# Kernel tuning notes

Measured on AMD Instinct MI355X. Metric: run time of the kernel, lower is better.

## Reference

```python
import jax, jax.numpy as jnp
import numpy as np

SIG = 10
C = 0.0
STD = 1.0
N_ATOMS = 21
N_TRAIN = 8192
DESC = N_ATOMS * (N_ATOMS - 1) // 2  # 210
M = 64


def setup_inputs() -> dict:
    key = jax.random.key(0)
    k1, k2, k3 = jax.random.split(key, 3)
    Rs = jax.random.normal(k1, (M, N_ATOMS, 3), dtype=jnp.float32)
    xs_train = jax.random.uniform(k2, (N_TRAIN, DESC), dtype=jnp.float32)
    Jx_alphas = jax.random.normal(k3, (N_TRAIN, DESC), dtype=jnp.float32)
    return {"Rs": Rs, "xs_train": xs_train, "Jx_alphas": Jx_alphas}


def reference(Rs, xs_train, Jx_alphas):
    sig = SIG
    q = np.sqrt(5.0) / sig
    n = N_ATOMS
    # pairwise atom displacements / distances: [M, n, n, 3], [M, n, n]
    diffs = Rs[:, :, None, :] - Rs[:, None, :, :]
    dists = jnp.linalg.norm(diffs, axis=-1)
    eye = jnp.eye(n, dtype=bool)
    dists = jnp.where(eye, jnp.inf, dists)  # kill diagonal
    i, j = np.tril_indices(n, k=-1)
    xs = 1.0 / dists[:, i, j]                       # [M, D] inverse-distance descriptor
    x_diffs = q * xs[:, None, :] - q * xs_train     # [M, T, D]
    x_dists = jnp.linalg.norm(x_diffs, axis=-1)     # [M, T]
    exp_xs = (5.0 / (3.0 * sig ** 2)) * jnp.exp(-x_dists)
    dot = jnp.einsum('mtd,td->mt', x_diffs, Jx_alphas)
    exp_xs_1 = exp_xs * (1.0 + x_dists)
    F1s_x = jnp.einsum('mt,mtd->md', exp_xs * dot, x_diffs)  # [M, D]
    F2s_x = exp_xs_1 @ Jx_alphas                              # [M, D]
    Fs_x = (F1s_x - F2s_x) * STD
    # expand_tril: scatter D lower-tri values to symmetric [M, n, n], zero diag
    full = jnp.zeros((Fs_x.shape[0], n, n), dtype=Fs_x.dtype)
    full = full.at[:, i, j].set(Fs_x).at[:, j, i].set(Fs_x)
    Fs = jnp.einsum('mab,mabc->mac', full / dists ** 3, diffs)  # diag: 0/inf -> 0
    Es = jnp.sum(exp_xs_1 * dot, axis=-1) / q
    Es = C + Es * STD
    return Es, Fs
```

## Files before the change

kernel.cpp:

```cpp
#include <hip/hip_runtime.h>
#include <math.h>

#define NA   21
#define NM   64
#define ND   210
#define DP   224
#define NT   8192
#define NCH  28
#define KS2  32

#define QC 0.22360679774997896f
#define KE 0.016666666666666666f

typedef short bf8 __attribute__((ext_vector_type(8)));
typedef float f4  __attribute__((ext_vector_type(4)));

#define O_XF   0u
#define O_JF   917504u
#define O_XFT  1835008u
#define O_JFT  2752512u
#define O_W1   3670016u
#define O_E1   3932160u
#define O_AF   4194304u
#define O_QG   4201472u
#define O_NTT  4215808u
#define O_CJ   4224000u
#define O_NX   4232192u
#define O_PB   4261056u
#define O_ESP  5178560u
#define O_WAP  5211328u

__device__ __forceinline__ unsigned short f2bf(float f) {
    unsigned u = __float_as_uint(f);
    u += 0x7fffu + ((u >> 16) & 1u);
    return (unsigned short)(u >> 16);
}
__device__ __forceinline__ float bf2f(unsigned short h) {
    return __uint_as_float((unsigned)h << 16);
}

__device__ __forceinline__ void d_to_ij(int d, int& i, int& j) {
    int ii = (int)((1.0f + sqrtf(1.0f + 8.0f * (float)d)) * 0.5f);
    while (ii * (ii - 1) / 2 > d) --ii;
    while ((ii + 1) * ii / 2 <= d) ++ii;
    i = ii;
    j = d - ii * (ii - 1) / 2;
}

__global__ __launch_bounds__(256) void k_prep(
    const float* __restrict__ Rs, const float* __restrict__ xs,
    const float* __restrict__ Jx,
    unsigned short* __restrict__ Xf, unsigned short* __restrict__ Jf,
    unsigned short* __restrict__ XfT, unsigned short* __restrict__ JfT,
    unsigned short* __restrict__ Af, float* __restrict__ qxsG,
    float* __restrict__ nx, float* __restrict__ nt, float* __restrict__ cJ) {
    const int b = blockIdx.x, tid = threadIdx.x;
    __shared__ float lds[2 * 16 * 210];

    if (b < 512) {
        const int t0 = b * 16;
        const float4* sx = (const float4*)(xs + (size_t)t0 * ND);
        const float4* sj = (const float4*)(Jx + (size_t)t0 * ND);
#pragma unroll
        for (int k = 0; k < 4; ++k) {
            const int i = k * 256 + tid;
            if (i < 840) {
                ((float4*)lds)[i] = sx[i];
                ((float4*)(lds + 3360))[i] = sj[i];
            }
        }
        __syncthreads();
#pragma unroll
        for (int k = 0; k < 7; ++k) {
            const int idx = k * 256 + tid;
            if (idx < 896) {
                const int arr = idx / 448;
                const int rem = idx - arr * 448;
                const int kq = rem >> 4, colt = rem & 15;
                const float* src = lds + arr * 3360 + colt * 210;
                const float sc = arr ? 1.0f : QC;
                union { unsigned short us[8]; uint4 v; } u;
#pragma unroll
                for (int i = 0; i < 8; ++i) {
                    const int d = kq * 8 + i;
                    u.us[i] = (d < ND) ? f2bf(sc * src[d]) : (unsigned short)0;
                }
                *(uint4*)((arr ? Jf : Xf) + ((size_t)(b * NCH + kq) * 16 + colt) * 8) = u.v;
            } else {
                const int idx2 = idx - 896;
                const int arr = idx2 / 448;
                const int rem = idx2 - arr * 448;
                const int dtile = rem >> 5;
                const int rem2 = rem & 31;
                const int tql = rem2 >> 4, col = rem2 & 15;
                const int d = dtile * 16 + col;
                const float* src = lds + arr * 3360 + tql * 8 * 210;
                const float sc = arr ? 1.0f : QC;
                union { unsigned short us[8]; uint4 v; } u;
#pragma unroll
                for (int i = 0; i < 8; ++i)
                    u.us[i] = (d < ND) ? f2bf(sc * src[i * 210 + d])
                                       : (unsigned short)0;
                const size_t off = ((size_t)(dtile * 1024 + b * 2 + tql) * 16 + col) * 8;
                *(uint4*)((arr ? JfT : XfT) + off) = u.v;
            }
        }
        const int tt = tid >> 4, l = tid & 15;
        const float* xr = lds + tt * 210;
        const float* jr = lds + 3360 + tt * 210;
        float sn = 0.0f, sc2 = 0.0f;
        for (int c = l; c < ND; c += 16) {
            float x = bf2f(f2bf(QC * xr[c]));
            float j = bf2f(f2bf(jr[c]));
            sn = fmaf(x, x, sn);
            sc2 = fmaf(x, j, sc2);
        }
#pragma unroll
        for (int off = 1; off < 16; off <<= 1) {
            sn += __shfl_xor(sn, off);
            sc2 += __shfl_xor(sc2, off);
        }
        if (l == 0) {
            nt[t0 + tt] = sn;
            cJ[t0 + tt] = sc2;
        }
    } else {
        const int m = b - 512;
        float* R = lds;
        float* red = lds + 64;
        if (tid < NA * 3) R[tid] = Rs[m * NA * 3 + tid];
        __syncthreads();
        float local = 0.0f;
        if (tid < DP) {
            float vr = 0.0f;
            unsigned short hv = 0;
            if (tid < ND) {
                int i, j; d_to_ij(tid, i, j);
                float dx = R[i * 3] - R[j * 3];
                float dy = R[i * 3 + 1] - R[j * 3 + 1];
                float dz = R[i * 3 + 2] - R[j * 3 + 2];
                float v = QC / sqrtf(dx * dx + dy * dy + dz * dz);
                hv = f2bf(v);
                vr = bf2f(hv);
            }
            Af[(((m >> 4) * NCH + (tid >> 3)) * 16 + (m & 15)) * 8 + (tid & 7)] = hv;
            qxsG[(tid >> 2) * 256 + m * 4 + (tid & 3)] = vr;
            local = vr * vr;
        }
        red[tid] = local;
        __syncthreads();
        for (int s = 128; s > 0; s >>= 1) {
            if (tid < s) red[tid] += red[tid + s];
            __syncthreads();
        }
        if (tid == 0) nx[m] = red[0];
    }
}

__global__ __launch_bounds__(256) void k_stage1(
    const unsigned short* __restrict__ Af, const unsigned short* __restrict__ Xf,
    const unsigned short* __restrict__ Jf, const float* __restrict__ nt,
    const float* __restrict__ cJ, const float* __restrict__ nx,
    unsigned short* __restrict__ w1f, unsigned short* __restrict__ e1f,
    float* __restrict__ EsPart, float* __restrict__ WaPart) {
    const int tid = threadIdx.x;
    const int lane = tid & 63;
    const int w = tid >> 6;
    const int col = lane & 15, quad = lane >> 4;
    const int ttile = blockIdx.x;
    __shared__ float Dw[64][17];
    __shared__ float De[64][17];

    const unsigned short* ap = Af + ((size_t)(w * NCH + quad) * 16 + col) * 8;
    const unsigned short* xp = Xf + ((size_t)(ttile * NCH + quad) * 16 + col) * 8;
    const unsigned short* jp = Jf + ((size_t)(ttile * NCH + quad) * 16 + col) * 8;

    bf8 af[7];
#pragma unroll
    for (int kc = 0; kc < 7; ++kc) af[kc] = *(const bf8*)(ap + kc * 512);

    bf8 bx[2], bj[2];
    bx[0] = *(const bf8*)xp;
    bj[0] = *(const bf8*)jp;
    bx[1] = *(const bf8*)(xp + 512);
    bj[1] = *(const bf8*)(jp + 512);

    f4 c1 = {0.f, 0.f, 0.f, 0.f};
    f4 c2 = {0.f, 0.f, 0.f, 0.f};
#pragma unroll
    for (int kc = 0; kc < 7; ++kc) {
        const int s = kc & 1;
        c1 = __builtin_amdgcn_mfma_f32_16x16x32_bf16(af[kc], bx[s], c1, 0, 0, 0);
        c2 = __builtin_amdgcn_mfma_f32_16x16x32_bf16(af[kc], bj[s], c2, 0, 0, 0);
        if (kc < 5) {
            bx[s] = *(const bf8*)(xp + (kc + 2) * 512);
            bj[s] = *(const bf8*)(jp + (kc + 2) * 512);
        }
    }

    const int t = ttile * 16 + col;
    const float ntv = nt[t], cjv = cJ[t];
    float esA[4], wlA[4];
#pragma unroll
    for (int r = 0; r < 4; ++r) {
        const int m = w * 16 + quad * 4 + r;
        float sq = fmaxf(nx[m] - 2.0f * c1[r] + ntv, 0.0f);
        float xd = sqrtf(sq);
        float e = KE * expf(-xd);
        float dotv = c2[r] - cjv;
        float wv = e * dotv;
        float ev = e * (1.0f + xd);
        Dw[m][col] = wv;
        De[m][col] = ev;
        esA[r] = ev * dotv;
        wlA[r] = wv;
    }
    __syncthreads();
    {
        const int aidx = tid >> 7;
        const int c = tid & 127;
        const int mtile = c >> 5, tql = (c >> 4) & 1, colm = c & 15;
        const float* srcD = aidx ? &De[0][0] : &Dw[0][0];
        unsigned short* dst = aidx ? e1f : w1f;
        const int m = mtile * 16 + colm;
        union { unsigned short us[8]; uint4 v; } u;
#pragma unroll
        for (int i = 0; i < 8; ++i) u.us[i] = f2bf(srcD[m * 17 + tql * 8 + i]);
        const size_t off = ((size_t)(mtile * 1024 + ttile * 2 + tql) * 16 + colm) * 8;
        *(uint4*)(dst + off) = u.v;
    }
#pragma unroll
    for (int r = 0; r < 4; ++r) {
        float e = esA[r], wl = wlA[r];
#pragma unroll
        for (int off = 1; off < 16; off <<= 1) {
            e += __shfl_xor(e, off);
            wl += __shfl_xor(wl, off);
        }
        if (col == 0) {
            const int m = w * 16 + quad * 4 + r;
            EsPart[(size_t)m * 512 + ttile] = e;
            WaPart[(size_t)m * 512 + ttile] = wl;
        }
    }
}

__global__ __launch_bounds__(256) void k_stage2(
    const unsigned short* __restrict__ w1f, const unsigned short* __restrict__ e1f,
    const unsigned short* __restrict__ XfT, const unsigned short* __restrict__ JfT,
    float* __restrict__ Pbuf) {
    const int tid = threadIdx.x;
    const int lane = tid & 63;
    const int w = tid >> 6;
    const int col = lane & 15, quad = lane >> 4;
    const int dt = blockIdx.x;
    const int by = blockIdx.y;

    const unsigned short* awp = w1f + ((size_t)(w * 1024 + by * 32 + quad) * 16 + col) * 8;
    const unsigned short* aep = e1f + ((size_t)(w * 1024 + by * 32 + quad) * 16 + col) * 8;
    const unsigned short* bxp = XfT + ((size_t)(dt * 1024 + by * 32 + quad) * 16 + col) * 8;
    const unsigned short* bjp = JfT + ((size_t)(dt * 1024 + by * 32 + quad) * 16 + col) * 8;

    bf8 aw[2], ae[2], bx[2], bj[2];
    aw[0] = *(const bf8*)awp;         ae[0] = *(const bf8*)aep;
    bx[0] = *(const bf8*)bxp;         bj[0] = *(const bf8*)bjp;
    aw[1] = *(const bf8*)(awp + 512); ae[1] = *(const bf8*)(aep + 512);
    bx[1] = *(const bf8*)(bxp + 512); bj[1] = *(const bf8*)(bjp + 512);

    f4 dA = {0.f, 0.f, 0.f, 0.f};
    f4 dB = {0.f, 0.f, 0.f, 0.f};
#pragma unroll
    for (int kk = 0; kk < 8; ++kk) {
        const int s = kk & 1;
        dA = __builtin_amdgcn_mfma_f32_16x16x32_bf16(aw[s], bx[s], dA, 0, 0, 0);
        dB = __builtin_amdgcn_mfma_f32_16x16x32_bf16(ae[s], bj[s], dB, 0, 0, 0);
        if (kk < 6) {
            aw[s] = *(const bf8*)(awp + (kk + 2) * 512);
            ae[s] = *(const bf8*)(aep + (kk + 2) * 512);
            bx[s] = *(const bf8*)(bxp + (kk + 2) * 512);
            bj[s] = *(const bf8*)(bjp + (kk + 2) * 512);
        }
    }
    float* p = Pbuf + (size_t)by * 28672 + dt * 16 + col;
#pragma unroll
    for (int r = 0; r < 4; ++r) {
        const int m = w * 16 + quad * 4 + r;
        p[m * DP] = dA[r];
        p[14336 + m * DP] = dB[r];
    }
}

__global__ void k_final(const float* __restrict__ Rs, const float* __restrict__ qxsG,
                        const float* __restrict__ Pbuf, const float* __restrict__ EsPart,
                        const float* __restrict__ WaPart, float* __restrict__ out) {
    int m = blockIdx.x, tid = threadIdx.x;
    __shared__ float R[NA * 3];
    __shared__ float Ff[NA][NA];
    __shared__ float redE[256];
    __shared__ float redW[256];
    __shared__ float ABs[DP];
    if (tid < NA * 3) R[tid] = Rs[m * NA * 3 + tid];
    if (tid < NA) Ff[tid][tid] = 0.0f;
    if (tid < DP) {
        const float* p0 = Pbuf + (size_t)m * DP + tid;
        float s1 = 0.0f, s2 = 0.0f;
#pragma unroll
        for (int ks = 0; ks < KS2; ++ks) {
            s1 += p0[(size_t)ks * 28672];
            s2 += p0[(size_t)ks * 28672 + 14336];
        }
        ABs[tid] = s1 + s2;
    }
    {
        const float2 ep = ((const float2*)(EsPart + (size_t)m * 512))[tid];
        const float2 wp = ((const float2*)(WaPart + (size_t)m * 512))[tid];
        redE[tid] = ep.x + ep.y;
        redW[tid] = wp.x + wp.y;
    }
    __syncthreads();
    for (int s = 128; s > 0; s >>= 1) {
        if (tid < s) {
            redE[tid] += redE[tid + s];
            redW[tid] += redW[tid + s];
        }
        __syncthreads();
    }
    const float Wa = redW[0];
    if (tid < ND) {
        int i, j; d_to_ij(tid, i, j);
        float dx = R[i * 3] - R[j * 3];
        float dy = R[i * 3 + 1] - R[j * 3 + 1];
        float dz = R[i * 3 + 2] - R[j * 3 + 2];
        float dist2 = dx * dx + dy * dy + dz * dz;
        float fsx = qxsG[(tid >> 2) * 256 + m * 4 + (tid & 3)] * Wa - ABs[tid];
        float f = fsx / (dist2 * sqrtf(dist2));
        Ff[i][j] = f;
        Ff[j][i] = f;
    }
    __syncthreads();
    if (tid < NA * 3) {
        int a = tid / 3, c = tid % 3;
        float s = 0.0f;
        for (int b = 0; b < NA; ++b) {
            if (b == a) continue;
            s += Ff[a][b] * (R[a * 3 + c] - R[b * 3 + c]);
        }
        out[NM + m * NA * 3 + tid] = s;
    }
    if (tid == 0) out[m] = redE[0] / QC;
}

extern "C" void kernel_launch(void* const* d_in, const int* in_sizes, int n_in,
                              void* d_out, int out_size, void* d_ws, size_t ws_size,
                              hipStream_t stream) {
    const float* Rs = (const float*)d_in[0];
    const float* xs_train = (const float*)d_in[1];
    const float* Jx_alphas = (const float*)d_in[2];
    float* out = (float*)d_out;
    float* ws = (float*)d_ws;

    unsigned short* Xf  = (unsigned short*)(ws + O_XF);
    unsigned short* Jf  = (unsigned short*)(ws + O_JF);
    unsigned short* XfT = (unsigned short*)(ws + O_XFT);
    unsigned short* JfT = (unsigned short*)(ws + O_JFT);
    unsigned short* w1f = (unsigned short*)(ws + O_W1);
    unsigned short* e1f = (unsigned short*)(ws + O_E1);
    unsigned short* Af  = (unsigned short*)(ws + O_AF);
    float* qxsG   = ws + O_QG;
    float* nt     = ws + O_NTT;
    float* cJ     = ws + O_CJ;
    float* nx     = ws + O_NX;
    float* Pbuf   = ws + O_PB;
    float* EsPart = ws + O_ESP;
    float* WaPart = ws + O_WAP;

    k_prep<<<576, 256, 0, stream>>>(Rs, xs_train, Jx_alphas, Xf, Jf, XfT, JfT,
                                    Af, qxsG, nx, nt, cJ);
    k_stage1<<<512, 256, 0, stream>>>(Af, Xf, Jf, nt, cJ, nx, w1f, e1f, EsPart, WaPart);
    k_stage2<<<dim3(14, KS2), 256, 0, stream>>>(w1f, e1f, XfT, JfT, Pbuf);
    k_final<<<NM, 256, 0, stream>>>(Rs, qxsG, Pbuf, EsPart, WaPart, out);
}
```

Before: 92.13 us.

## Fuse prep and stage1 kernels, recomputing descriptor fragments per block in LDS

Merges the preprocessing kernel into stage1. Each block recomputes the full 64-molecule inverse-distance A-fragments and its own train-tile bf16 B-fragments in shared memory, instead of writing them to global workspace and reading them back. This removes one kernel launch and the global round trip for Xf/Jf/Af/nt/cJ/nx, and k_final now recomputes qxs itself. The cost is redundant work: every one of the 512 blocks reads all of Rs and recomputes 64x224 inverse distances, and the larger LDS footprint may lower occupancy.

Result: slower. 105.3 us (+14.2%).

```diff
diff --git a/kernel.cpp b/kernel.cpp
--- a/kernel.cpp
+++ b/kernel.cpp
@@ -15,17 +15,10 @@
 typedef short bf8 __attribute__((ext_vector_type(8)));
 typedef float f4  __attribute__((ext_vector_type(4)));
 
-#define O_XF   0u
-#define O_JF   917504u
 #define O_XFT  1835008u
 #define O_JFT  2752512u
 #define O_W1   3670016u
 #define O_E1   3932160u
-#define O_AF   4194304u
-#define O_QG   4201472u
-#define O_NTT  4215808u
-#define O_CJ   4224000u
-#define O_NX   4232192u
 #define O_PB   4261056u
 #define O_ESP  5178560u
 #define O_WAP  5211328u
@@ -47,120 +40,10 @@
     j = d - ii * (ii - 1) / 2;
 }
 
-__global__ __launch_bounds__(256) void k_prep(
+__global__ __launch_bounds__(256) void k_mega(
     const float* __restrict__ Rs, const float* __restrict__ xs,
     const float* __restrict__ Jx,
-    unsigned short* __restrict__ Xf, unsigned short* __restrict__ Jf,
     unsigned short* __restrict__ XfT, unsigned short* __restrict__ JfT,
-    unsigned short* __restrict__ Af, float* __restrict__ qxsG,
-    float* __restrict__ nx, float* __restrict__ nt, float* __restrict__ cJ) {
-    const int b = blockIdx.x, tid = threadIdx.x;
-    __shared__ float lds[2 * 16 * 210];
-
-    if (b < 512) {
-        const int t0 = b * 16;
-        const float4* sx = (const float4*)(xs + (size_t)t0 * ND);
-        const float4* sj = (const float4*)(Jx + (size_t)t0 * ND);
-#pragma unroll
-        for (int k = 0; k < 4; ++k) {
-            const int i = k * 256 + tid;
-            if (i < 840) {
-                ((float4*)lds)[i] = sx[i];
-                ((float4*)(lds + 3360))[i] = sj[i];
-            }
-        }
-        __syncthreads();
-#pragma unroll
-        for (int k = 0; k < 7; ++k) {
-            const int idx = k * 256 + tid;
-            if (idx < 896) {
-                const int arr = idx / 448;
-                const int rem = idx - arr * 448;
-                const int kq = rem >> 4, colt = rem & 15;
-                const float* src = lds + arr * 3360 + colt * 210;
-                const float sc = arr ? 1.0f : QC;
-                union { unsigned short us[8]; uint4 v; } u;
-#pragma unroll
-                for (int i = 0; i < 8; ++i) {
-                    const int d = kq * 8 + i;
-                    u.us[i] = (d < ND) ? f2bf(sc * src[d]) : (unsigned short)0;
-                }
-                *(uint4*)((arr ? Jf : Xf) + ((size_t)(b * NCH + kq) * 16 + colt) * 8) = u.v;
-            } else {
-                const int idx2 = idx - 896;
-                const int arr = idx2 / 448;
-                const int rem = idx2 - arr * 448;
-                const int dtile = rem >> 5;
-                const int rem2 = rem & 31;
-                const int tql = rem2 >> 4, col = rem2 & 15;
-                const int d = dtile * 16 + col;
-                const float* src = lds + arr * 3360 + tql * 8 * 210;
-                const float sc = arr ? 1.0f : QC;
-                union { unsigned short us[8]; uint4 v; } u;
-#pragma unroll
-                for (int i = 0; i < 8; ++i)
-                    u.us[i] = (d < ND) ? f2bf(sc * src[i * 210 + d])
-                                       : (unsigned short)0;
-                const size_t off = ((size_t)(dtile * 1024 + b * 2 + tql) * 16 + col) * 8;
-                *(uint4*)((arr ? JfT : XfT) + off) = u.v;
-            }
-        }
-        const int tt = tid >> 4, l = tid & 15;
-        const float* xr = lds + tt * 210;
-        const float* jr = lds + 3360 + tt * 210;
-        float sn = 0.0f, sc2 = 0.0f;
-        for (int c = l; c < ND; c += 16) {
-            float x = bf2f(f2bf(QC * xr[c]));
-            float j = bf2f(f2bf(jr[c]));
-            sn = fmaf(x, x, sn);
-            sc2 = fmaf(x, j, sc2);
-        }
-#pragma unroll
-        for (int off = 1; off < 16; off <<= 1) {
-            sn += __shfl_xor(sn, off);
-            sc2 += __shfl_xor(sc2, off);
-        }
-        if (l == 0) {
-            nt[t0 + tt] = sn;
-            cJ[t0 + tt] = sc2;
-        }
-    } else {
-        const int m = b - 512;
-        float* R = lds;
-        float* red = lds + 64;
-        if (tid < NA * 3) R[tid] = Rs[m * NA * 3 + tid];
-        __syncthreads();
-        float local = 0.0f;
-        if (tid < DP) {
-            float vr = 0.0f;
-            unsigned short hv = 0;
-            if (tid < ND) {
-                int i, j; d_to_ij(tid, i, j);
-                float dx = R[i * 3] - R[j * 3];
-                float dy = R[i * 3 + 1] - R[j * 3 + 1];
-                float dz = R[i * 3 + 2] - R[j * 3 + 2];
-                float v = QC / sqrtf(dx * dx + dy * dy + dz * dz);
-                hv = f2bf(v);
-                vr = bf2f(hv);
-            }
-            Af[(((m >> 4) * NCH + (tid >> 3)) * 16 + (m & 15)) * 8 + (tid & 7)] = hv;
-            qxsG[(tid >> 2) * 256 + m * 4 + (tid & 3)] = vr;
-            local = vr * vr;
-        }
-        red[tid] = local;
-        __syncthreads();
-        for (int s = 128; s > 0; s >>= 1) {
-            if (tid < s) red[tid] += red[tid + s];
-            __syncthreads();
-        }
-        if (tid == 0) nx[m] = red[0];
-    }
-}
-
-__global__ __launch_bounds__(256) void k_stage1(
-    const unsigned short* __restrict__ Af, const unsigned short* __restrict__ Xf,
-    const unsigned short* __restrict__ Jf, const float* __restrict__ nt,
-    const float* __restrict__ cJ, const float* __restrict__ nx,
     unsigned short* __restrict__ w1f, unsigned short* __restrict__ e1f,
     float* __restrict__ EsPart, float* __restrict__ WaPart) {
     const int tid = threadIdx.x;
@@ -168,59 +51,177 @@
     const int w = tid >> 6;
     const int col = lane & 15, quad = lane >> 4;
     const int ttile = blockIdx.x;
-    __shared__ float Dw[64][17];
-    __shared__ float De[64][17];
-
-    const unsigned short* ap = Af + ((size_t)(w * NCH + quad) * 16 + col) * 8;
-    const unsigned short* xp = Xf + ((size_t)(ttile * NCH + quad) * 16 + col) * 8;
-    const unsigned short* jp = Jf + ((size_t)(ttile * NCH + quad) * 16 + col) * 8;
-
-    bf8 af[7];
-#pragma unroll
-    for (int kc = 0; kc < 7; ++kc) af[kc] = *(const bf8*)(ap + kc * 512);
-
-    bf8 bx[2], bj[2];
-    bx[0] = *(const bf8*)xp;
-    bj[0] = *(const bf8*)jp;
-    bx[1] = *(const bf8*)(xp + 512);
-    bj[1] = *(const bf8*)(jp + 512);
+    const int t0 = ttile * 16;
+
+    __shared__ float lds[17680];
+    float* stage = lds;
+    unsigned short* Bfr = (unsigned short*)(lds + 6720);
+    unsigned short* Afr = (unsigned short*)(lds + 10304);
+    unsigned short* ijt = (unsigned short*)(lds + 17472);
+    float* ntL = lds + 17584;
+    float* cJL = lds + 17600;
+    float* nxL = lds + 17616;
+
+#pragma unroll
+    for (int k = 0; k < 16; ++k) {
+        const int i = k * 256 + tid;
+        if (i < NM * NA * 3) stage[i] = Rs[i];
+    }
+    if (tid < DP) {
+        unsigned short v = 0;
+        if (tid < ND) {
+            int i, j; d_to_ij(tid, i, j);
+            v = (unsigned short)((i << 8) | j);
+        }
+        ijt[tid] = v;
+    }
+    __syncthreads();
+
+    for (int c = 0; c < 56; ++c) {
+        const int flat = c * 256 + tid;
+        const int i8 = flat & 7;
+        const int colm = (flat >> 3) & 15;
+        const int rest = flat >> 7;
+        const int wm = rest / 28, kq = rest - wm * 28;
+        const int m = wm * 16 + colm, d = kq * 8 + i8;
+        unsigned short hv = 0;
+        if (d < ND) {
+            const int pij = ijt[d];
+            const int pi = pij >> 8, pj = pij & 255;
+            const float* Rm = stage + m * 63;
+            const float dx = Rm[pi * 3]     - Rm[pj * 3];
+            const float dy = Rm[pi * 3 + 1] - Rm[pj * 3 + 1];
+            const float dz = Rm[pi * 3 + 2] - Rm[pj * 3 + 2];
+            hv = f2bf(QC / sqrtf(dx * dx + dy * dy + dz * dz));
+        }
+        Afr[flat] = hv;
+    }
+    __syncthreads();
+
+    {
+        const float4* sx = (const float4*)(xs + (size_t)t0 * ND);
+        const float4* sj = (const float4*)(Jx + (size_t)t0 * ND);
+#pragma unroll
+        for (int k = 0; k < 4; ++k) {
+            const int i = k * 256 + tid;
+            if (i < 840) {
+                ((float4*)stage)[i] = sx[i];
+                ((float4*)(stage + 3360))[i] = sj[i];
+            }
+        }
+    }
+    __syncthreads();
+
+#pragma unroll
+    for (int k = 0; k < 7; ++k) {
+        const int idx = k * 256 + tid;
+        if (idx < 896) {
+            const int arr = idx / 448;
+            const int rem = idx - arr * 448;
+            const int kq = rem >> 4, colt = rem & 15;
+            const float* src = stage + arr * 3360 + colt * 210;
+            const float sc = arr ? 1.0f : QC;
+            union { unsigned short us[8]; uint4 v; } u;
+#pragma unroll
+            for (int i = 0; i < 8; ++i) {
+                const int d = kq * 8 + i;
+                u.us[i] = (d < ND) ? f2bf(sc * src[d]) : (unsigned short)0;
+            }
+            *(uint4*)(Bfr + (size_t)arr * 3584 + ((size_t)kq * 16 + colt) * 8) = u.v;
+        } else {
+            const int idx2 = idx - 896;
+            const int arr = idx2 / 448;
+            const int rem = idx2 - arr * 448;
+            const int dtile = rem >> 5;
+            const int rem2 = rem & 31;
+            const int tql = rem2 >> 4, c2 = rem2 & 15;
+            const int d = dtile * 16 + c2;
+            const float* src = stage + arr * 3360 + tql * 8 * 210;
+            const float sc = arr ? 1.0f : QC;
+            union { unsigned short us[8]; uint4 v; } u;
+#pragma unroll
+            for (int i = 0; i < 8; ++i)
+                u.us[i] = (d < ND) ? f2bf(sc * src[i * 210 + d]) : (unsigned short)0;
+            const size_t off = ((size_t)(dtile * 1024 + ttile * 2 + tql) * 16 + c2) * 8;
+            *(uint4*)((arr ? JfT : XfT) + off) = u.v;
+        }
+    }
+    {
+        const int tt = tid >> 4, l = tid & 15;
+        const float* xr = stage + tt * 210;
+        const float* jr = stage + 3360 + tt * 210;
+        float sn = 0.0f, sc2 = 0.0f;
+        for (int c = l; c < ND; c += 16) {
+            const float x = bf2f(f2bf(QC * xr[c]));
+            const float j = bf2f(f2bf(jr[c]));
+            sn = fmaf(x, x, sn);
+            sc2 = fmaf(x, j, sc2);
+        }
+#pragma unroll
+        for (int off = 1; off < 16; off <<= 1) {
+            sn += __shfl_xor(sn, off);
+            sc2 += __shfl_xor(sc2, off);
+        }
+        if (l == 0) {
+            ntL[tt] = sn;
+            cJL[tt] = sc2;
+        }
+    }
+    {
+        float sn = 0.0f;
+#pragma unroll
+        for (int kk = 0; kk < 7; ++kk) {
+            const int kq = quad + kk * 4;
+            const unsigned short* a = Afr + ((size_t)(w * NCH + kq) * 16 + col) * 8;
+#pragma unroll
+            for (int i = 0; i < 8; ++i) {
+                const float v = bf2f(a[i]);
+                sn = fmaf(v, v, sn);
+            }
+        }
+        sn += __shfl_xor(sn, 16);
+        sn += __shfl_xor(sn, 32);
+        if (quad == 0) nxL[w * 16 + col] = sn;
+    }
+    __syncthreads();
 
     f4 c1 = {0.f, 0.f, 0.f, 0.f};
-    f4 c2 = {0.f, 0.f, 0.f, 0.f};
+    f4 c2v = {0.f, 0.f, 0.f, 0.f};
 #pragma unroll
     for (int kc = 0; kc < 7; ++kc) {
-        const int s = kc & 1;
-        c1 = __builtin_amdgcn_mfma_f32_16x16x32_bf16(af[kc], bx[s], c1, 0, 0, 0);
-        c2 = __builtin_amdgcn_mfma_f32_16x16x32_bf16(af[kc], bj[s], c2, 0, 0, 0);
-        if (kc < 5) {
-            bx[s] = *(const bf8*)(xp + (kc + 2) * 512);
-            bj[s] = *(const bf8*)(jp + (kc + 2) * 512);
-        }
-    }
-
-    const int t = ttile * 16 + col;
-    const float ntv = nt[t], cjv = cJ[t];
+        const int kq = kc * 4 + quad;
+        const bf8 a  = *(const bf8*)(Afr + ((size_t)(w * NCH + kq) * 16 + col) * 8);
+        const bf8 bx = *(const bf8*)(Bfr + ((size_t)kq * 16 + col) * 8);
+        const bf8 bj = *(const bf8*)(Bfr + 3584 + ((size_t)kq * 16 + col) * 8);
+        c1  = __builtin_amdgcn_mfma_f32_16x16x32_bf16(a, bx, c1, 0, 0, 0);
+        c2v = __builtin_amdgcn_mfma_f32_16x16x32_bf16(a, bj, c2v, 0, 0, 0);
+    }
+
+    float* Dw = stage;
+    float* De = stage + 1088;
+    const float ntv = ntL[col], cjv = cJL[col];
     float esA[4], wlA[4];
 #pragma unroll
     for (int r = 0; r < 4; ++r) {
         const int m = w * 16 + quad * 4 + r;
-        float sq = fmaxf(nx[m] - 2.0f * c1[r] + ntv, 0.0f);
-        float xd = sqrtf(sq);
-        float e = KE * expf(-xd);
-        float dotv = c2[r] - cjv;
-        float wv = e * dotv;
-        float ev = e * (1.0f + xd);
-        Dw[m][col] = wv;
-        De[m][col] = ev;
+        const float sq = fmaxf(nxL[m] - 2.0f * c1[r] + ntv, 0.0f);
+        const float xd = sqrtf(sq);
+        const float e = KE * expf(-xd);
+        const float dotv = c2v[r] - cjv;
+        const float wv = e * dotv;
+        const float ev = e * (1.0f + xd);
+        Dw[m * 17 + col] = wv;
+        De[m * 17 + col] = ev;
         esA[r] = ev * dotv;
         wlA[r] = wv;
     }
     __syncthreads();
+
     {
         const int aidx = tid >> 7;
         const int c = tid & 127;
         const int mtile = c >> 5, tql = (c >> 4) & 1, colm = c & 15;
-        const float* srcD = aidx ? &De[0][0] : &Dw[0][0];
+        const float* srcD = aidx ? De : Dw;
         unsigned short* dst = aidx ? e1f : w1f;
         const int m = mtile * 16 + colm;
         union { unsigned short us[8]; uint4 v; } u;
@@ -290,7 +291,7 @@
     }
 }
 
-__global__ void k_final(const float* __restrict__ Rs, const float* __restrict__ qxsG,
+__global__ void k_final(const float* __restrict__ Rs,
                         const float* __restrict__ Pbuf, const float* __restrict__ EsPart,
                         const float* __restrict__ WaPart, float* __restrict__ out) {
     int m = blockIdx.x, tid = threadIdx.x;
@@ -332,7 +333,8 @@
         float dy = R[i * 3 + 1] - R[j * 3 + 1];
         float dz = R[i * 3 + 2] - R[j * 3 + 2];
         float dist2 = dx * dx + dy * dy + dz * dz;
-        float fsx = qxsG[(tid >> 2) * 256 + m * 4 + (tid & 3)] * Wa - ABs[tid];
+        float qxs = bf2f(f2bf(QC / sqrtf(dist2)));
+        float fsx = qxs * Wa - ABs[tid];
         float f = fsx / (dist2 * sqrtf(dist2));
         Ff[i][j] = f;
         Ff[j][i] = f;
@@ -359,24 +361,16 @@
     float* out = (float*)d_out;
     float* ws = (float*)d_ws;
 
-    unsigned short* Xf  = (unsigned short*)(ws + O_XF);
-    unsigned short* Jf  = (unsigned short*)(ws + O_JF);
     unsigned short* XfT = (unsigned short*)(ws + O_XFT);
     unsigned short* JfT = (unsigned short*)(ws + O_JFT);
     unsigned short* w1f = (unsigned short*)(ws + O_W1);
     unsigned short* e1f = (unsigned short*)(ws + O_E1);
-    unsigned short* Af  = (unsigned short*)(ws + O_AF);
-    float* qxsG   = ws + O_QG;
-    float* nt     = ws + O_NTT;
-    float* cJ     = ws + O_CJ;
-    float* nx     = ws + O_NX;
     float* Pbuf   = ws + O_PB;
     float* EsPart = ws + O_ESP;
     float* WaPart = ws + O_WAP;
 
-    k_prep<<<576, 256, 0, stream>>>(Rs, xs_train, Jx_alphas, Xf, Jf, XfT, JfT,
-                                    Af, qxsG, nx, nt, cJ);
-    k_stage1<<<512, 256, 0, stream>>>(Af, Xf, Jf, nt, cJ, nx, w1f, e1f, EsPart, WaPart);
+    k_mega<<<512, 256, 0, stream>>>(Rs, xs_train, Jx_alphas, XfT, JfT,
+                                    w1f, e1f, EsPart, WaPart);
     k_stage2<<<dim3(14, KS2), 256, 0, stream>>>(w1f, e1f, XfT, JfT, Pbuf);
-    k_final<<<NM, 256, 0, stream>>>(Rs, qxsG, Pbuf, EsPart, WaPart, out);
-}
+    k_final<<<NM, 256, 0, stream>>>(Rs, Pbuf, EsPart, WaPart, out);
+}
```
